# Kernel optimization log

Measured on AMD Instinct MI355X. Metric: run time of the kernel, lower is better.

The kernel has to match this reference:

```python
import jax, jax.numpy as jnp
import numpy as np

N_NODES = 100000
N_EDGES = 1600000
N_GRAPHS = 64
D_IN = 128
D_HID = 128
D_OUT = 4
LEAKY_SLOPE = 0.01  # nn.LeakyReLU default


def setup_inputs() -> dict:
    key = jax.random.key(0)
    k1, k2, k3, k4, k5 = jax.random.split(key, 5)
    x = jax.random.normal(k1, (N_NODES, D_IN), dtype=jnp.float32)
    edge_index = jax.random.randint(k2, (2, N_EDGES), 0, N_NODES, dtype=jnp.int32)
    batch = jnp.sort(jax.random.randint(k3, (N_NODES,), 0, N_GRAPHS, dtype=jnp.int32))
    s1 = 1.0 / np.sqrt(D_IN)
    W1 = jax.random.uniform(k4, (D_IN, D_HID), jnp.float32, -s1, s1)
    b1 = jnp.zeros((D_HID,), jnp.float32)
    W2 = jax.random.uniform(k5, (D_HID, D_OUT), jnp.float32, -s1, s1)
    b2 = jnp.zeros((D_OUT,), jnp.float32)
    return {"x": x, "edge_index": edge_index, "batch": batch,
            "W1": W1, "b1": b1, "W2": W2, "b2": b2}


def _gcn_conv(x, src, dst, norm, W, b, n_nodes):
    # h = X W; messages = norm * h[src]; aggregate at dst; add bias
    h = x @ W
    msg = h[src] * norm[:, None]
    agg = jax.ops.segment_sum(msg, dst, num_segments=n_nodes)
    return agg + b


def reference(x, edge_index, batch, W1, b1, W2, b2):
    n = x.shape[0]
    # add self-loops (PyG GCNConv default)
    loops = jnp.arange(n, dtype=edge_index.dtype)
    src = jnp.concatenate([edge_index[0], loops])
    dst = jnp.concatenate([edge_index[1], loops])
    # symmetric normalization: deg over target index, weight 1
    deg = jax.ops.segment_sum(jnp.ones_like(src, dtype=x.dtype), dst, num_segments=n)
    deg_is = jnp.where(deg > 0, jax.lax.rsqrt(deg), 0.0)
    norm = deg_is[src] * deg_is[dst]

    h = _gcn_conv(x, src, dst, norm, W1, b1, n)
    h = jnp.where(h >= 0, h, LEAKY_SLOPE * h)  # LeakyReLU
    # dropout is identity at inference
    h = _gcn_conv(h, src, dst, norm, W2, b2, n)

    # global mean pool over graphs
    sums = jax.ops.segment_sum(h, batch, num_segments=N_GRAPHS)
    cnts = jax.ops.segment_sum(jnp.ones((n,), h.dtype), batch, num_segments=N_GRAPHS)
    pooled = sums / jnp.maximum(cnts, 1.0)[:, None]
    return jax.nn.softmax(pooled, axis=1)
```

## Files before the change

### kernel.cpp

```cpp
#include <hip/hip_runtime.h>

#define D 128
#define NG 64
#define NPB 256
#define MAXBK 512
#define CAPB 8192
#define PCHUNK 2048
#define PLCAP 5376
#define ENTCAP 21
#define NPASS 4
#define LDA 136

typedef unsigned int uint;
typedef unsigned short ushort_t;
typedef unsigned char uchar_t;
typedef float v2f __attribute__((ext_vector_type(2)));
typedef short s8v __attribute__((ext_vector_type(8)));
typedef float f4v __attribute__((ext_vector_type(4)));

__device__ __forceinline__ uint bfr(float x) {
    uint u = __float_as_uint(x);
    return (u + 0x7FFFu + ((u >> 16) & 1u)) >> 16;
}

__global__ __launch_bounds__(256) void k_init(const float* __restrict__ W,
                                              short* __restrict__ W1T,
                                              int* __restrict__ gcur, int NBK) {
    int idx = blockIdx.x * 256 + threadIdx.x;
    int nn = idx >> 7, kk = idx & 127;
    W1T[idx] = (short)bfr(W[kk * D + nn]);
    if (idx < NBK) gcur[idx] = idx * CAPB;
}

__global__ __launch_bounds__(256) void k_part(const int* __restrict__ edge,
                                              int* __restrict__ gcur, int* __restrict__ p1,
                                              int E, int NBK) {
    __shared__ int hist[MAXBK], scn[MAXBK], curb[MAXBK], fixb[MAXBK];
    __shared__ int ps[256];
    __shared__ int sortb[PCHUNK];
    __shared__ ushort_t sbkt[PCHUNK];
    int tid = threadIdx.x;
    for (int i = tid; i < MAXBK; i += 256) { hist[i] = 0; curb[i] = 0; }
    __syncthreads();
    int lo = blockIdx.x * PCHUNK;
    int hi = min(lo + PCHUNK, E);
    int cnt = hi - lo;
    for (int e = lo + tid; e < hi; e += 256) atomicAdd(&hist[edge[E + e] >> 8], 1);
    __syncthreads();
    int a = hist[2 * tid], b = hist[2 * tid + 1];
    ps[tid] = a + b;
    __syncthreads();
    for (int o = 1; o < 256; o <<= 1) {
        int x = (tid >= o) ? ps[tid - o] : 0;
        __syncthreads();
        ps[tid] += x;
        __syncthreads();
    }
    int pe = ps[tid] - (a + b);
    scn[2 * tid] = pe;
    scn[2 * tid + 1] = pe + a;
    __syncthreads();
    for (int bk = tid; bk < NBK; bk += 256)
        if (hist[bk]) fixb[bk] = atomicAdd(&gcur[bk], hist[bk]) - scn[bk];
    __syncthreads();
    for (int e = lo + tid; e < hi; e += 256) {
        int s = edge[e];
        int d2 = edge[E + e];
        int bk = d2 >> 8;
        int r = scn[bk] + atomicAdd(&curb[bk], 1);
        sortb[r] = ((d2 & 255) << 17) | s;
        sbkt[r] = (ushort_t)bk;
    }
    __syncthreads();
    for (int p = tid; p < cnt; p += 256) {
        int bk = sbkt[p];
        p1[fixb[bk] + p] = sortb[p];
    }
}

__global__ __launch_bounds__(256) void k_place(const int* __restrict__ p1,
                                               const int* __restrict__ gcur,
                                               int* __restrict__ ed, int2* __restrict__ offdeg,
                                               float* __restrict__ dinv, int n) {
    __shared__ int cnts[256], scn[256], cur[256];
    __shared__ int outb[PLCAP];
    __shared__ int tot;
    int tid = threadIdx.x;
    int b = blockIdx.x;
    int base = b * CAPB;
    int cnt = gcur[b] - base;
    int end = base + cnt;
    int node0 = b << 8;
    cnts[tid] = 0;
    cur[tid] = 0;
    __syncthreads();
    int ent[ENTCAP];
    int ne = 0;
    for (int p = base + tid; p < end; p += 256) {
        int v = p1[p];
        if (ne < ENTCAP) ent[ne] = v;
        ne++;
        atomicAdd(&cnts[v >> 17], 1);
    }
    __syncthreads();
    int v0 = cnts[tid];
    int pc = (v0 + 3) & ~3;
    scn[tid] = pc;
    __syncthreads();
    for (int o = 1; o < 256; o <<= 1) {
        int x = (tid >= o) ? scn[tid - o] : 0;
        __syncthreads();
        scn[tid] += x;
        __syncthreads();
    }
    int excl = scn[tid] - pc;
    if (tid == 255) tot = scn[255];
    int node = node0 + tid;
    if (node < n) {
        offdeg[node] = make_int2(base + excl, v0);
        dinv[node] = rsqrtf((float)(v0 + 1));
    }
    scn[tid] = excl;
    __syncthreads();
    int m = (ne < ENTCAP) ? ne : ENTCAP;
    for (int k = 0; k < m; ++k) {
        int v = ent[k];
        int l = v >> 17;
        int r = scn[l] + atomicAdd(&cur[l], 1);
        if (r < PLCAP) outb[r] = v & 0x1FFFF;
        else ed[base + r] = v & 0x1FFFF;
    }
    for (int p = base + tid + ENTCAP * 256; p < end; p += 256) {
        int v = p1[p];
        int l = v >> 17;
        int r = scn[l] + atomicAdd(&cur[l], 1);
        if (r < PLCAP) outb[r] = v & 0x1FFFF;
        else ed[base + r] = v & 0x1FFFF;
    }
    __syncthreads();
    int lim = (tot < PLCAP) ? tot : PLCAP;
    for (int p = tid; p < lim; p += 256) ed[base + p] = outb[p];
}

__global__ __launch_bounds__(256) void k_gemm_mfma(const float* __restrict__ X,
                                                   const short* __restrict__ W1T,
                                                   const float* __restrict__ dinv,
                                                   uchar_t* __restrict__ H8b, int M) {
    __shared__ short sA[128 * LDA];
    __shared__ short sB[128 * LDA];
    __shared__ float sDinv[128];
    const int tid = threadIdx.x;
    const int blockM = blockIdx.x * 128;

    if (tid < 128) {
        int gm = blockM + tid;
        sDinv[tid] = (gm < M) ? dinv[gm] : 0.f;
    }
    {
        int c = tid & 31, g = tid >> 5;
#pragma unroll
        for (int i = 0; i < 16; ++i) {
            int r = g + i * 8;
            int gm = blockM + r;
            float4 v = make_float4(0, 0, 0, 0);
            if (gm < M) v = *(const float4*)&X[(size_t)gm * D + c * 4];
            uint lo = bfr(v.x) | (bfr(v.y) << 16);
            uint hi = bfr(v.z) | (bfr(v.w) << 16);
            *(uint2*)&sA[r * LDA + c * 4] = make_uint2(lo, hi);
        }
    }
    {
        int nn = tid >> 1, seg = tid & 1;
        const short* src = W1T + nn * 128 + seg * 64;
        short* dst = &sB[nn * LDA + seg * 64];
#pragma unroll
        for (int i = 0; i < 8; ++i)
            *(int4*)&dst[i * 8] = *(const int4*)&src[i * 8];
    }
    __syncthreads();

    const int wv = tid >> 6;
    const int lane = tid & 63;
    const int m0w = (wv >> 1) * 64, n0w = (wv & 1) * 64;
    const int mrow = lane & 15;
    const int quad = lane >> 4;

    f4v acc[4][4];
#pragma unroll
    for (int mi = 0; mi < 4; ++mi)
#pragma unroll
        for (int ni = 0; ni < 4; ++ni) acc[mi][ni] = (f4v)(0.f);

#pragma unroll
    for (int ks = 0; ks < 4; ++ks) {
        s8v af[4], bf[4];
#pragma unroll
        for (int mi = 0; mi < 4; ++mi)
            af[mi] = *(const s8v*)&sA[(m0w + mi * 16 + mrow) * LDA + ks * 32 + quad * 8];
#pragma unroll
        for (int ni = 0; ni < 4; ++ni)
            bf[ni] = *(const s8v*)&sB[(n0w + ni * 16 + mrow) * LDA + ks * 32 + quad * 8];
#pragma unroll
        for (int mi = 0; mi < 4; ++mi)
#pragma unroll
            for (int ni = 0; ni < 4; ++ni)
                acc[mi][ni] = __builtin_amdgcn_mfma_f32_16x16x32_bf16(af[mi], bf[ni], acc[mi][ni], 0, 0, 0);
    }

#pragma unroll
    for (int mi = 0; mi < 4; ++mi) {
#pragma unroll
        for (int r = 0; r < 4; ++r) {
            int lrow = m0w + mi * 16 + quad * 4 + r;
            int gm = blockM + lrow;
            if (gm >= M) continue;
            float di = sDinv[lrow];
#pragma unroll
            for (int ni = 0; ni < 4; ++ni) {
                int col = n0w + ni * 16 + mrow;
                float v = acc[mi][ni][r] * di;
                uint p = __builtin_amdgcn_cvt_pk_fp8_f32(v, v, 0u, false);
                H8b[((size_t)(col >> 5) * M + gm) * 32 + (col & 31)] = (uchar_t)(p & 0xFF);
            }
        }
    }
}

__device__ __forceinline__ void acc16(float* acc, uint4 r) {
    uint u[4] = {r.x, r.y, r.z, r.w};
#pragma unroll
    for (int q = 0; q < 4; ++q) {
        v2f lo = __builtin_amdgcn_cvt_pk_f32_fp8(u[q], false);
        v2f hi = __builtin_amdgcn_cvt_pk_f32_fp8(u[q], true);
        acc[4 * q + 0] += lo.x;
        acc[4 * q + 1] += lo.y;
        acc[4 * q + 2] += hi.x;
        acc[4 * q + 3] += hi.y;
    }
}

__global__ __launch_bounds__(256) void k_gather(const uint* __restrict__ Hsu,
                                                const int2* __restrict__ offdeg,
                                                const int* __restrict__ ed,
                                                const float* __restrict__ dinv,
                                                const float* __restrict__ b1,
                                                const float* __restrict__ W2,
                                                float4* __restrict__ zpart,
                                                int n) {
    __shared__ float sW[128];
    __shared__ float sb[32];
    int tid = threadIdx.x;
    int p = blockIdx.x & 3;
    if (tid < 128) sW[tid] = W2[p * 128 + tid];
    if (tid < 32) sb[tid] = b1[p * 32 + tid];
    __syncthreads();
    int node = (blockIdx.x >> 2) * 128 + (tid >> 1);
    if (node >= n) return;
    int lane = tid & 1;
    const uint4* T = (const uint4*)Hsu + (size_t)p * n * 2;
    float di = dinv[node];
    float acc[16];
    {
        uint4 h = T[(node << 1) + lane];
        uint u[4] = {h.x, h.y, h.z, h.w};
#pragma unroll
        for (int q = 0; q < 4; ++q) {
            v2f lo = __builtin_amdgcn_cvt_pk_f32_fp8(u[q], false);
            v2f hi = __builtin_amdgcn_cvt_pk_f32_fp8(u[q], true);
            acc[4 * q + 0] = lo.x;
            acc[4 * q + 1] = lo.y;
            acc[4 * q + 2] = hi.x;
            acc[4 * q + 3] = hi.y;
        }
    }
    int2 od = offdeg[node];
    int j = od.x, j1 = od.x + od.y;
    for (; j + 8 <= j1; j += 8) {
        int4 e0 = *(const int4*)&ed[j];
        int4 e1 = *(const int4*)&ed[j + 4];
        uint4 r0 = T[(e0.x << 1) + lane];
        uint4 r1 = T[(e0.y << 1) + lane];
        uint4 r2 = T[(e0.z << 1) + lane];
        uint4 r3 = T[(e0.w << 1) + lane];
        uint4 r4 = T[(e1.x << 1) + lane];
        uint4 r5 = T[(e1.y << 1) + lane];
        uint4 r6 = T[(e1.z << 1) + lane];
        uint4 r7 = T[(e1.w << 1) + lane];
        acc16(acc, r0); acc16(acc, r1); acc16(acc, r2); acc16(acc, r3);
        acc16(acc, r4); acc16(acc, r5); acc16(acc, r6); acc16(acc, r7);
    }
    if (j + 4 <= j1) {
        int4 e0 = *(const int4*)&ed[j];
        uint4 r0 = T[(e0.x << 1) + lane];
        uint4 r1 = T[(e0.y << 1) + lane];
        uint4 r2 = T[(e0.z << 1) + lane];
        uint4 r3 = T[(e0.w << 1) + lane];
        acc16(acc, r0); acc16(acc, r1); acc16(acc, r2); acc16(acc, r3);
        j += 4;
    }
    for (; j < j1; ++j) {
        uint4 r = T[(ed[j] << 1) + lane];
        acc16(acc, r);
    }
    int f = lane * 16;
    float a0 = 0.f, a1 = 0.f, a2 = 0.f, a3 = 0.f;
#pragma unroll
    for (int i = 0; i < 16; ++i) {
        float v = di * acc[i] + sb[f + i];
        v = v >= 0.f ? v : 0.01f * v;
        const float* w = &sW[(f + i) * 4];
        a0 += v * w[0];
        a1 += v * w[1];
        a2 += v * w[2];
        a3 += v * w[3];
    }
    a0 += __shfl_xor(a0, 1);
    a1 += __shfl_xor(a1, 1);
    a2 += __shfl_xor(a2, 1);
    a3 += __shfl_xor(a3, 1);
    if (lane == 0) zpart[(size_t)p * n + node] = make_float4(a0, a1, a2, a3);
}

__global__ __launch_bounds__(256) void k_zred(const float4* __restrict__ zpart,
                                              const float* __restrict__ dinv,
                                              float4* __restrict__ zs,
                                              float* __restrict__ psum,
                                              float* __restrict__ pcnt, int n) {
    int tid = threadIdx.x;
    if (blockIdx.x == 0) {
        if (tid < NG * 4) psum[tid] = 0.f;
        if (tid < NG) pcnt[tid] = 0.f;
    }
    int i = blockIdx.x * 256 + tid;
    if (i >= n) return;
    float4 a = zpart[i];
    float4 b = zpart[(size_t)n + i];
    float4 c = zpart[(size_t)2 * n + i];
    float4 d = zpart[(size_t)3 * n + i];
    float di = dinv[i];
    zs[i] = make_float4(di * (a.x + b.x + c.x + d.x), di * (a.y + b.y + c.y + d.y),
                        di * (a.z + b.z + c.z + d.z), di * (a.w + b.w + c.w + d.w));
}

__global__ __launch_bounds__(256) void k_pool2(const int* __restrict__ p1,
                                               const int* __restrict__ gcur,
                                               const float4* __restrict__ zs,
                                               const float* __restrict__ dinv,
                                               const int* __restrict__ batch,
                                               float* __restrict__ psum, float* __restrict__ pcnt,
                                               int n) {
    __shared__ float ls[NG * 4];
    __shared__ float lc[NG];
    __shared__ float dinvd[NPB];
    __shared__ int gl[NPB];
    int tid = threadIdx.x;
    int b = blockIdx.x >> 2;
    int qtr = blockIdx.x & 3;
    int node0 = b << 8;
    int node = node0 + tid;
    ls[tid] = 0.f;
    if (tid < NG) lc[tid] = 0.f;
    bool valid = node < n;
    float di = valid ? dinv[node] : 0.f;
    int g = valid ? batch[node] : -1;
    dinvd[tid] = di;
    gl[tid] = g;
    __syncthreads();
    float a0 = 0.f, a1 = 0.f, a2 = 0.f, a3 = 0.f;
    int cg = -1;
    if (qtr == 0 && valid) {
        float4 zv = zs[node];
        cg = g;
        a0 = di * zv.x; a1 = di * zv.y; a2 = di * zv.z; a3 = di * zv.w;
        atomicAdd(&lc[g], 1.f);
    }
    int base = b * CAPB;
    int cnt = gcur[b] - base;
    int s0 = base + ((cnt * qtr) >> 2);
    int s1 = base + ((cnt * (qtr + 1)) >> 2);
    for (int p = s0 + tid; p < s1; p += 1024) {
        int vv[4];
        float4 zb[4];
        int nb = 0;
#pragma unroll
        for (int k = 0; k < 4; ++k) {
            int q = p + k * 256;
            if (q < s1) vv[nb++] = p1[q];
        }
#pragma unroll
        for (int k = 0; k < 4; ++k)
            if (k < nb) zb[k] = zs[vv[k] & 0x1FFFF];
#pragma unroll
        for (int k = 0; k < 4; ++k) {
            if (k >= nb) continue;
            int dl = vv[k] >> 17;
            float w = dinvd[dl];
            int eg = gl[dl];
            if (eg != cg) {
                if (cg >= 0) {
                    atomicAdd(&ls[cg * 4 + 0], a0);
                    atomicAdd(&ls[cg * 4 + 1], a1);
                    atomicAdd(&ls[cg * 4 + 2], a2);
                    atomicAdd(&ls[cg * 4 + 3], a3);
                }
                cg = eg;
                a0 = a1 = a2 = a3 = 0.f;
            }
            a0 += w * zb[k].x; a1 += w * zb[k].y; a2 += w * zb[k].z; a3 += w * zb[k].w;
        }
    }
    if (cg >= 0) {
        atomicAdd(&ls[cg * 4 + 0], a0);
        atomicAdd(&ls[cg * 4 + 1], a1);
        atomicAdd(&ls[cg * 4 + 2], a2);
        atomicAdd(&ls[cg * 4 + 3], a3);
    }
    __syncthreads();
    atomicAdd(&psum[tid], ls[tid]);
    if (tid < NG) atomicAdd(&pcnt[tid], lc[tid]);
}

__global__ void k_final(const float* __restrict__ psum, const float* __restrict__ pcnt,
                        const float* __restrict__ b2, float* __restrict__ out) {
    int g = threadIdx.x;
    float c = fmaxf(pcnt[g], 1.f);
    float inv = 1.f / c;
    float l0 = psum[g * 4 + 0] * inv + b2[0];
    float l1 = psum[g * 4 + 1] * inv + b2[1];
    float l2 = psum[g * 4 + 2] * inv + b2[2];
    float l3 = psum[g * 4 + 3] * inv + b2[3];
    float m = fmaxf(fmaxf(l0, l1), fmaxf(l2, l3));
    float e0 = expf(l0 - m), e1 = expf(l1 - m), e2 = expf(l2 - m), e3 = expf(l3 - m);
    float s = 1.f / (e0 + e1 + e2 + e3);
    *(float4*)&out[g * 4] = make_float4(e0 * s, e1 * s, e2 * s, e3 * s);
}

extern "C" void kernel_launch(void* const* d_in, const int* in_sizes, int n_in,
                              void* d_out, int out_size, void* d_ws, size_t ws_size,
                              hipStream_t stream) {
    const float* X = (const float*)d_in[0];
    const int* edge = (const int*)d_in[1];
    const int* batch = (const int*)d_in[2];
    const float* W1 = (const float*)d_in[3];
    const float* b1 = (const float*)d_in[4];
    const float* W2 = (const float*)d_in[5];
    const float* b2 = (const float*)d_in[6];
    float* out = (float*)d_out;
    const int n = in_sizes[2];
    const int E = in_sizes[1] / 2;
    const int NBK = (n + NPB - 1) / NPB;

    uint* Hs = (uint*)d_ws;
    int* p1 = (int*)(Hs + (size_t)n * 32);
    int* ed = p1 + (size_t)NBK * CAPB;
    float4* zpart = (float4*)(ed + (size_t)NBK * CAPB);
    float4* zs = zpart + (size_t)NPASS * n;
    float* dinv = (float*)(zs + n);
    int2* offdeg = (int2*)(dinv + n);
    short* W1T = (short*)(offdeg + n);
    int* gcur = (int*)(W1T + 16384);
    float* psum = (float*)(gcur + MAXBK);
    float* pcnt = psum + NG * 4;

    const int NP = (E + PCHUNK - 1) / PCHUNK;
    const int NGB = (n + 127) / 128;

    k_init<<<64, 256, 0, stream>>>(W1, W1T, gcur, NBK);
    k_part<<<NP, 256, 0, stream>>>(edge, gcur, p1, E, NBK);
    k_place<<<NBK, 256, 0, stream>>>(p1, gcur, ed, offdeg, dinv, n);

    k_gemm_mfma<<<(n + 127) / 128, 256, 0, stream>>>(X, W1T, dinv, (uchar_t*)Hs, n);

    k_gather<<<NGB * NPASS, 256, 0, stream>>>(Hs, offdeg, ed, dinv, b1, W2, zpart, n);
    k_zred<<<(n + 255) / 256, 256, 0, stream>>>(zpart, dinv, zs, psum, pcnt, n);

    k_pool2<<<NBK * 4, 256, 0, stream>>>(p1, gcur, zs, dinv, batch, psum, pcnt, n);
    k_final<<<1, 64, 0, stream>>>(psum, pcnt, b2, out);
}
```

Measured before the change: 259.3 us.

## Gather full fp8 rows per node with 32-lane warps, drop partial-sum reduction kernel

The fp8 hidden matrix is now stored row-major, 128 bytes per node, instead of split into four 32-column slabs. The gather kernel now assigns 32 lanes to each node, so one pass reads full rows. The lanes reduce the W2 projection with shuffles and write the final z directly. This removes the four-pass layout, the zpart buffer and the k_zred kernel, and moves the psum/pcnt zeroing into k_init. It also changes partition chunk size and pool split from quarters to halves, trading parallelism in those kernels for fewer blocks; per-edge loads become 4-byte per lane coalesced 128B rows.

```diff
diff --git a/kernel.cpp b/kernel.cpp
--- a/kernel.cpp
+++ b/kernel.cpp
@@ -5,10 +5,9 @@
 #define NPB 256
 #define MAXBK 512
 #define CAPB 8192
-#define PCHUNK 2048
+#define PCHUNK 4096
 #define PLCAP 5376
 #define ENTCAP 21
-#define NPASS 4
 #define LDA 136
 
 typedef unsigned int uint;
@@ -25,11 +24,18 @@
 
 __global__ __launch_bounds__(256) void k_init(const float* __restrict__ W,
                                               short* __restrict__ W1T,
-                                              int* __restrict__ gcur, int NBK) {
-    int idx = blockIdx.x * 256 + threadIdx.x;
+                                              int* __restrict__ gcur,
+                                              float* __restrict__ psum,
+                                              float* __restrict__ pcnt, int NBK) {
+    int tid = threadIdx.x;
+    int idx = blockIdx.x * 256 + tid;
     int nn = idx >> 7, kk = idx & 127;
     W1T[idx] = (short)bfr(W[kk * D + nn]);
     if (idx < NBK) gcur[idx] = idx * CAPB;
+    if (blockIdx.x == 0) {
+        psum[tid] = 0.f;
+        if (tid < NG) pcnt[tid] = 0.f;
+    }
 }
 
 __global__ __launch_bounds__(256) void k_part(const int* __restrict__ edge,
@@ -220,126 +226,98 @@
                 int col = n0w + ni * 16 + mrow;
                 float v = acc[mi][ni][r] * di;
                 uint p = __builtin_amdgcn_cvt_pk_fp8_f32(v, v, 0u, false);
-                H8b[((size_t)(col >> 5) * M + gm) * 32 + (col & 31)] = (uchar_t)(p & 0xFF);
+                H8b[(size_t)gm * 128 + col] = (uchar_t)(p & 0xFF);
             }
         }
     }
 }
 
-__device__ __forceinline__ void acc16(float* acc, uint4 r) {
-    uint u[4] = {r.x, r.y, r.z, r.w};
-#pragma unroll
-    for (int q = 0; q < 4; ++q) {
-        v2f lo = __builtin_amdgcn_cvt_pk_f32_fp8(u[q], false);
-        v2f hi = __builtin_amdgcn_cvt_pk_f32_fp8(u[q], true);
-        acc[4 * q + 0] += lo.x;
-        acc[4 * q + 1] += lo.y;
-        acc[4 * q + 2] += hi.x;
-        acc[4 * q + 3] += hi.y;
-    }
-}
-
-__global__ __launch_bounds__(256) void k_gather(const uint* __restrict__ Hsu,
+__device__ __forceinline__ void acc4(float& c0, float& c1, float& c2, float& c3, uint r) {
+    v2f lo = __builtin_amdgcn_cvt_pk_f32_fp8(r, false);
+    v2f hi = __builtin_amdgcn_cvt_pk_f32_fp8(r, true);
+    c0 += lo.x; c1 += lo.y; c2 += hi.x; c3 += hi.y;
+}
+
+__global__ __launch_bounds__(256) void k_gather(const uint* __restrict__ T,
                                                 const int2* __restrict__ offdeg,
                                                 const int* __restrict__ ed,
                                                 const float* __restrict__ dinv,
                                                 const float* __restrict__ b1,
                                                 const float* __restrict__ W2,
-                                                float4* __restrict__ zpart,
+                                                float4* __restrict__ zs,
                                                 int n) {
-    __shared__ float sW[128];
-    __shared__ float sb[32];
     int tid = threadIdx.x;
-    int p = blockIdx.x & 3;
-    if (tid < 128) sW[tid] = W2[p * 128 + tid];
-    if (tid < 32) sb[tid] = b1[p * 32 + tid];
-    __syncthreads();
-    int node = (blockIdx.x >> 2) * 128 + (tid >> 1);
+    int node = blockIdx.x * 8 + (tid >> 5);
     if (node >= n) return;
-    int lane = tid & 1;
-    const uint4* T = (const uint4*)Hsu + (size_t)p * n * 2;
+    int lane = tid & 31;
+    int f = lane * 4;
     float di = dinv[node];
-    float acc[16];
+    float c0, c1, c2, c3;
     {
-        uint4 h = T[(node << 1) + lane];
-        uint u[4] = {h.x, h.y, h.z, h.w};
-#pragma unroll
-        for (int q = 0; q < 4; ++q) {
-            v2f lo = __builtin_amdgcn_cvt_pk_f32_fp8(u[q], false);
-            v2f hi = __builtin_amdgcn_cvt_pk_f32_fp8(u[q], true);
-            acc[4 * q + 0] = lo.x;
-            acc[4 * q + 1] = lo.y;
-            acc[4 * q + 2] = hi.x;
-            acc[4 * q + 3] = hi.y;
-        }
+        uint h = T[(node << 5) + lane];
+        v2f lo = __builtin_amdgcn_cvt_pk_f32_fp8(h, false);
+        v2f hi = __builtin_amdgcn_cvt_pk_f32_fp8(h, true);
+        c0 = lo.x; c1 = lo.y; c2 = hi.x; c3 = hi.y;
+    }
+    float w[4][4], bb[4];
+#pragma unroll
+    for (int i = 0; i < 4; ++i) {
+        bb[i] = b1[f + i];
+#pragma unroll
+        for (int k = 0; k < 4; ++k) w[i][k] = W2[(f + i) * 4 + k];
     }
     int2 od = offdeg[node];
     int j = od.x, j1 = od.x + od.y;
     for (; j + 8 <= j1; j += 8) {
         int4 e0 = *(const int4*)&ed[j];
         int4 e1 = *(const int4*)&ed[j + 4];
-        uint4 r0 = T[(e0.x << 1) + lane];
-        uint4 r1 = T[(e0.y << 1) + lane];
-        uint4 r2 = T[(e0.z << 1) + lane];
-        uint4 r3 = T[(e0.w << 1) + lane];
-        uint4 r4 = T[(e1.x << 1) + lane];
-        uint4 r5 = T[(e1.y << 1) + lane];
-        uint4 r6 = T[(e1.z << 1) + lane];
-        uint4 r7 = T[(e1.w << 1) + lane];
-        acc16(acc, r0); acc16(acc, r1); acc16(acc, r2); acc16(acc, r3);
-        acc16(acc, r4); acc16(acc, r5); acc16(acc, r6); acc16(acc, r7);
+        uint r0 = T[(e0.x << 5) + lane];
+        uint r1 = T[(e0.y << 5) + lane];
+        uint r2 = T[(e0.z << 5) + lane];
+        uint r3 = T[(e0.w << 5) + lane];
+        uint r4 = T[(e1.x << 5) + lane];
+        uint r5 = T[(e1.y << 5) + lane];
+        uint r6 = T[(e1.z << 5) + lane];
+        uint r7 = T[(e1.w << 5) + lane];
+        acc4(c0, c1, c2, c3, r0); acc4(c0, c1, c2, c3, r1);
+        acc4(c0, c1, c2, c3, r2); acc4(c0, c1, c2, c3, r3);
+        acc4(c0, c1, c2, c3, r4); acc4(c0, c1, c2, c3, r5);
+        acc4(c0, c1, c2, c3, r6); acc4(c0, c1, c2, c3, r7);
     }
     if (j + 4 <= j1) {
         int4 e0 = *(const int4*)&ed[j];
-        uint4 r0 = T[(e0.x << 1) + lane];
-        uint4 r1 = T[(e0.y << 1) + lane];
-        uint4 r2 = T[(e0.z << 1) + lane];
-        uint4 r3 = T[(e0.w << 1) + lane];
-        acc16(acc, r0); acc16(acc, r1); acc16(acc, r2); acc16(acc, r3);
+        uint r0 = T[(e0.x << 5) + lane];
+        uint r1 = T[(e0.y << 5) + lane];
+        uint r2 = T[(e0.z << 5) + lane];
+        uint r3 = T[(e0.w << 5) + lane];
+        acc4(c0, c1, c2, c3, r0); acc4(c0, c1, c2, c3, r1);
+        acc4(c0, c1, c2, c3, r2); acc4(c0, c1, c2, c3, r3);
         j += 4;
     }
     for (; j < j1; ++j) {
-        uint4 r = T[(ed[j] << 1) + lane];
-        acc16(acc, r);
-    }
-    int f = lane * 16;
-    float a0 = 0.f, a1 = 0.f, a2 = 0.f, a3 = 0.f;
-#pragma unroll
-    for (int i = 0; i < 16; ++i) {
-        float v = di * acc[i] + sb[f + i];
-        v = v >= 0.f ? v : 0.01f * v;
-        const float* w = &sW[(f + i) * 4];
-        a0 += v * w[0];
-        a1 += v * w[1];
-        a2 += v * w[2];
-        a3 += v * w[3];
-    }
-    a0 += __shfl_xor(a0, 1);
-    a1 += __shfl_xor(a1, 1);
-    a2 += __shfl_xor(a2, 1);
-    a3 += __shfl_xor(a3, 1);
-    if (lane == 0) zpart[(size_t)p * n + node] = make_float4(a0, a1, a2, a3);
-}
-
-__global__ __launch_bounds__(256) void k_zred(const float4* __restrict__ zpart,
-                                              const float* __restrict__ dinv,
-                                              float4* __restrict__ zs,
-                                              float* __restrict__ psum,
-                                              float* __restrict__ pcnt, int n) {
-    int tid = threadIdx.x;
-    if (blockIdx.x == 0) {
-        if (tid < NG * 4) psum[tid] = 0.f;
-        if (tid < NG) pcnt[tid] = 0.f;
-    }
-    int i = blockIdx.x * 256 + tid;
-    if (i >= n) return;
-    float4 a = zpart[i];
-    float4 b = zpart[(size_t)n + i];
-    float4 c = zpart[(size_t)2 * n + i];
-    float4 d = zpart[(size_t)3 * n + i];
-    float di = dinv[i];
-    zs[i] = make_float4(di * (a.x + b.x + c.x + d.x), di * (a.y + b.y + c.y + d.y),
-                        di * (a.z + b.z + c.z + d.z), di * (a.w + b.w + c.w + d.w));
+        uint r = T[(ed[j] << 5) + lane];
+        acc4(c0, c1, c2, c3, r);
+    }
+    float v0 = di * c0 + bb[0];
+    float v1 = di * c1 + bb[1];
+    float v2 = di * c2 + bb[2];
+    float v3 = di * c3 + bb[3];
+    v0 = v0 >= 0.f ? v0 : 0.01f * v0;
+    v1 = v1 >= 0.f ? v1 : 0.01f * v1;
+    v2 = v2 >= 0.f ? v2 : 0.01f * v2;
+    v3 = v3 >= 0.f ? v3 : 0.01f * v3;
+    float a0 = v0 * w[0][0] + v1 * w[1][0] + v2 * w[2][0] + v3 * w[3][0];
+    float a1 = v0 * w[0][1] + v1 * w[1][1] + v2 * w[2][1] + v3 * w[3][1];
+    float a2 = v0 * w[0][2] + v1 * w[1][2] + v2 * w[2][2] + v3 * w[3][2];
+    float a3 = v0 * w[0][3] + v1 * w[1][3] + v2 * w[2][3] + v3 * w[3][3];
+#pragma unroll
+    for (int o = 16; o >= 1; o >>= 1) {
+        a0 += __shfl_xor(a0, o);
+        a1 += __shfl_xor(a1, o);
+        a2 += __shfl_xor(a2, o);
+        a3 += __shfl_xor(a3, o);
+    }
+    if (lane == 0) zs[node] = make_float4(di * a0, di * a1, di * a2, di * a3);
 }
 
 __global__ __launch_bounds__(256) void k_pool2(const int* __restrict__ p1,
@@ -354,8 +332,8 @@
     __shared__ float dinvd[NPB];
     __shared__ int gl[NPB];
     int tid = threadIdx.x;
-    int b = blockIdx.x >> 2;
-    int qtr = blockIdx.x & 3;
+    int b = blockIdx.x >> 1;
+    int half = blockIdx.x & 1;
     int node0 = b << 8;
     int node = node0 + tid;
     ls[tid] = 0.f;
@@ -368,7 +346,7 @@
     __syncthreads();
     float a0 = 0.f, a1 = 0.f, a2 = 0.f, a3 = 0.f;
     int cg = -1;
-    if (qtr == 0 && valid) {
+    if (half == 0 && valid) {
         float4 zv = zs[node];
         cg = g;
         a0 = di * zv.x; a1 = di * zv.y; a2 = di * zv.z; a3 = di * zv.w;
@@ -376,8 +354,9 @@
     }
     int base = b * CAPB;
     int cnt = gcur[b] - base;
-    int s0 = base + ((cnt * qtr) >> 2);
-    int s1 = base + ((cnt * (qtr + 1)) >> 2);
+    int mid = cnt >> 1;
+    int s0 = base + (half ? mid : 0);
+    int s1 = base + (half ? cnt : mid);
     for (int p = s0 + tid; p < s1; p += 1024) {
         int vv[4];
         float4 zb[4];
@@ -453,8 +432,7 @@
     uint* Hs = (uint*)d_ws;
     int* p1 = (int*)(Hs + (size_t)n * 32);
     int* ed = p1 + (size_t)NBK * CAPB;
-    float4* zpart = (float4*)(ed + (size_t)NBK * CAPB);
-    float4* zs = zpart + (size_t)NPASS * n;
+    float4* zs = (float4*)(ed + (size_t)NBK * CAPB);
     float* dinv = (float*)(zs + n);
     int2* offdeg = (int2*)(dinv + n);
     short* W1T = (short*)(offdeg + n);
@@ -463,17 +441,16 @@
     float* pcnt = psum + NG * 4;
 
     const int NP = (E + PCHUNK - 1) / PCHUNK;
-    const int NGB = (n + 127) / 128;
-
-    k_init<<<64, 256, 0, stream>>>(W1, W1T, gcur, NBK);
+    const int NGB = (n + 7) / 8;
+
+    k_init<<<64, 256, 0, stream>>>(W1, W1T, gcur, psum, pcnt, NBK);
     k_part<<<NP, 256, 0, stream>>>(edge, gcur, p1, E, NBK);
     k_place<<<NBK, 256, 0, stream>>>(p1, gcur, ed, offdeg, dinv, n);
 
     k_gemm_mfma<<<(n + 127) / 128, 256, 0, stream>>>(X, W1T, dinv, (uchar_t*)Hs, n);
 
-    k_gather<<<NGB * NPASS, 256, 0, stream>>>(Hs, offdeg, ed, dinv, b1, W2, zpart, n);
-    k_zred<<<(n + 255) / 256, 256, 0, stream>>>(zpart, dinv, zs, psum, pcnt, n);
-
-    k_pool2<<<NBK * 4, 256, 0, stream>>>(p1, gcur, zs, dinv, batch, psum, pcnt, n);
+    k_gather<<<NGB, 256, 0, stream>>>(Hs, offdeg, ed, dinv, b1, W2, zs, n);
+
+    k_pool2<<<NBK * 2, 256, 0, stream>>>(p1, gcur, zs, dinv, batch, psum, pcnt, n);
     k_final<<<1, 64, 0, stream>>>(psum, pcnt, b2, out);
 }
```

New measurement: 227.7 us. -12.2%, faster.
